# Performance work log

Hardware: AMD Instinct MI355X
Metric: run time of the kernel (lower is better)

## Reference

```python
import jax, jax.numpy as jnp
import numpy as np

B, N, HID, NH = 16, 200, 64, 2
D = HID // NH
EPS = 1e-12
LOG_EPS = 1e-24


def setup_inputs() -> dict:
    key = jax.random.key(0)
    ks = jax.random.split(key, 24)
    r = lambda k, shp, s=1.0: (jax.random.normal(k, shp, dtype=jnp.float32) * s)
    inp = {
        "input_tensor": r(ks[0], (B, N, HID), 0.5),
        "attention_mask": jnp.zeros((B, 1, N, N), jnp.float32),
        "absolute_pos_K": r(ks[1], (B, N, HID), 0.5),
        "absolute_pos_V": r(ks[2], (B, N, HID), 0.5),
        "time_matrix_emb_K": r(ks[3], (B, N, N, HID), 0.1),
        "time_matrix_emb_V": r(ks[4], (B, N, N, HID), 0.1),
        # learned params (torch nn.Linear convention: y = x @ W.T + b)
        "Wq": r(ks[5], (HID, HID), 0.02), "bq": jnp.zeros((HID,), jnp.float32),
        "Wk": r(ks[6], (HID, HID), 0.02), "bk": jnp.zeros((HID,), jnp.float32),
        "Wv": r(ks[7], (HID, HID), 0.02), "bv": jnp.zeros((HID,), jnp.float32),
        "Wd": r(ks[8], (HID, HID), 0.02), "bd": jnp.zeros((HID,), jnp.float32),
        "order_w": r(ks[9], (2 * D,), 0.02), "order_b": jnp.zeros((1,), jnp.float32),
        "dist_w": r(ks[10], (2 * D,), 0.02), "dist_b": jnp.zeros((1,), jnp.float32),
        "scalar": r(ks[11], (1,)),
        "ln_g": jnp.ones((HID,), jnp.float32), "ln_b": jnp.zeros((HID,), jnp.float32),
    }
    return inp


def _split_heads(x):  # [B,N,HID] -> [B,NH,N,D]
    return x.reshape(B, N, NH, D).transpose(0, 2, 1, 3)


def reference(input_tensor, attention_mask, absolute_pos_K, absolute_pos_V,
              time_matrix_emb_K, time_matrix_emb_V,
              Wq, bq, Wk, bk, Wv, bv, Wd, bd,
              order_w, order_b, dist_w, dist_b, scalar, ln_g, ln_b):
    q = _split_heads(input_tensor @ Wq.T + bq)   # [B,H,N,D]
    k = _split_heads(input_tensor @ Wk.T + bk)
    v = _split_heads(input_tensor @ Wv.T + bv)
    pk = _split_heads(absolute_pos_K)
    pv = _split_heads(absolute_pos_V)
    tk = time_matrix_emb_K.reshape(B, N, N, NH, D).transpose(0, 3, 1, 2, 4)  # [B,H,N,N,D]
    tv = time_matrix_emb_V.reshape(B, N, N, NH, D).transpose(0, 3, 1, 2, 4)

    scores = jnp.einsum('bhid,bhjd->bhij', q, k)
    scores = scores + jnp.einsum('bhid,bhjd->bhij', q, pk)
    scores = scores + jnp.einsum('bhijd,bhid->bhij', tk, q)

    # order term: order_affine(cat(q_i, k_j)) decomposes as q_i.w1 + k_j.w2 + b,
    # so we never materialize the [B,H,N,N,2D] q_k tensor.
    logit_o = (jnp.einsum('bhid,d->bhi', q, order_w[:D])[..., :, None]
               + jnp.einsum('bhjd,d->bhj', k, order_w[D:])[..., None, :]
               + order_b[0])
    pr_order = jax.nn.sigmoid(logit_o)
    gd_order = jnp.triu(jnp.ones((N, N), jnp.float32), 1)  # 1 where j > i
    err_order = (jnp.log(pr_order + LOG_EPS) * gd_order
                 + jnp.log(1.0 - pr_order + LOG_EPS) * (1.0 - gd_order))

    # distance term (same decomposition)
    pr_dist = (jnp.einsum('bhid,d->bhi', q, dist_w[:D])[..., :, None]
               + jnp.einsum('bhjd,d->bhj', k, dist_w[D:])[..., None, :]
               + dist_b[0])
    idx = jnp.arange(N)
    gd_dist = jnp.log(jnp.abs(idx[None, :] - idx[:, None]).astype(jnp.float32) + 1.0)
    err_dist = -jnp.square(gd_dist - pr_dist) * jnp.square(scalar[0]) * 0.5

    scores = (scores + err_order + err_dist) / np.sqrt(D).astype(np.float32)
    scores = scores + attention_mask
    probs = jax.nn.softmax(scores, axis=-1)  # dropout is identity in eval mode

    ctx = (jnp.einsum('bhij,bhjd->bhid', probs, v)
           + jnp.einsum('bhij,bhjd->bhid', probs, pv)
           + jnp.einsum('bhij,bhijd->bhid', probs, tv))
    ctx = ctx.transpose(0, 2, 1, 3).reshape(B, N, HID)

    h = ctx @ Wd.T + bd + input_tensor
    mu = h.mean(-1, keepdims=True)
    var = jnp.square(h - mu).mean(-1, keepdims=True)
    return (h - mu) / jnp.sqrt(var + EPS) * ln_g + ln_b
```

## Files before the change

kernel.cpp:

```cpp
#include <hip/hip_runtime.h>
#include <math.h>

#define B 16
#define N 200
#define HID 64
#define NH 2
#define D 32
#define EPSF 1e-12f
#define LOG_EPSF 1e-24f

#define RSQRT_D 0.17677669529663687f

__global__ __launch_bounds__(256) void k_proj(
    const float* __restrict__ x,
    const float* __restrict__ pk,
    const float* __restrict__ pv,
    const float* __restrict__ Wq, const float* __restrict__ bq,
    const float* __restrict__ Wk, const float* __restrict__ bk,
    const float* __restrict__ Wv, const float* __restrict__ bv,
    const float* __restrict__ order_w, const float* __restrict__ dist_w,
    float* __restrict__ q,
    float* __restrict__ kp,
    float* __restrict__ vp,
    float* __restrict__ qo, float* __restrict__ ko,
    float* __restrict__ qd, float* __restrict__ kd)
{
    __shared__ float sX[4][HID];
    const int tid = threadIdx.x;
    const int sub = tid >> 6;
    const int o   = tid & 63;
    const int row = blockIdx.x * 4 + sub;

    sX[sub][o] = x[row * HID + o];
    __syncthreads();

    float qv = bq[o], kv = bk[o], vv = bv[o];
    #pragma unroll 8
    for (int c = 0; c < HID; ++c) {
        const float xv = sX[sub][c];
        qv = fmaf(xv, Wq[o * HID + c], qv);
        kv = fmaf(xv, Wk[o * HID + c], kv);
        vv = fmaf(xv, Wv[o * HID + c], vv);
    }
    q [row * HID + o] = qv;
    kp[row * HID + o] = kv + pk[row * HID + o];
    vp[row * HID + o] = vv + pv[row * HID + o];

    const int d = o & 31;
    float qov = qv * order_w[d];
    float kov = kv * order_w[D + d];
    float qdv = qv * dist_w[d];
    float kdv = kv * dist_w[D + d];
    #pragma unroll
    for (int m = 16; m >= 1; m >>= 1) {
        qov += __shfl_xor(qov, m);
        kov += __shfl_xor(kov, m);
        qdv += __shfl_xor(qdv, m);
        kdv += __shfl_xor(kdv, m);
    }
    if (d == 0) {
        const int bb = row / N;
        const int ii = row - bb * N;
        const int h  = o >> 5;
        const int idx = (bb * NH + h) * N + ii;
        qo[idx] = qov;  ko[idx] = kov;
        qd[idx] = qdv;  kd[idx] = kdv;
    }
}

__global__ __launch_bounds__(128) void k_attn(
    const float* __restrict__ q, const float* __restrict__ kp,
    const float* __restrict__ vp,
    const float* __restrict__ tk,
    const float* __restrict__ tv,
    const float* __restrict__ amask,
    const float* __restrict__ qo, const float* __restrict__ ko,
    const float* __restrict__ qd, const float* __restrict__ kd,
    const float* __restrict__ order_b, const float* __restrict__ dist_b,
    const float* __restrict__ scalar,
    float* __restrict__ ctx)
{
    __shared__ float sS[2][256];

    const int tid  = threadIdx.x;
    const int h    = tid >> 6;
    const int lane = tid & 63;
    const int g    = lane >> 3;
    const int c    = lane & 7;
    const int bi   = blockIdx.x;
    const int b    = bi / N;
    const int i    = bi - b * N;
    const int bh   = b * NH + h;

    float* S = sS[h];

    const float4 qf = ((const float4*)(q + (size_t)bi * HID + h * D))[c];

    const float qoi = qo[bh * N + i];
    const float qdi = qd[bh * N + i];
    const float ob  = order_b[0];
    const float db  = dist_b[0];
    const float sc  = scalar[0];
    const float sc2h = 0.5f * sc * sc;

    const float* kpb = kp + (size_t)b * N * HID + h * D;
    const float* tkb = tk + (size_t)bi * N * HID + h * D;
    const float* vpb = vp + (size_t)b * N * HID + h * D;
    const float* tvb = tv + (size_t)bi * N * HID + h * D;
    const float* mb  = amask + (size_t)bi * N;
    const float* kob = ko + (size_t)bh * N;
    const float* kdb = kd + (size_t)bh * N;

    #pragma unroll 5
    for (int it = 0; it < 25; ++it) {
        const int j = it * 8 + g;
        const float4 kv  = ((const float4*)(kpb + (size_t)j * HID))[c];
        const float4 tkv = ((const float4*)(tkb + (size_t)j * HID))[c];
        float part = qf.x * (kv.x + tkv.x) + qf.y * (kv.y + tkv.y)
                   + qf.z * (kv.z + tkv.z) + qf.w * (kv.w + tkv.w);
        part += __shfl_xor(part, 1);
        part += __shfl_xor(part, 2);
        part += __shfl_xor(part, 4);

        const float lo = qoi + kob[j] + ob;
        const float pr = 1.0f / (1.0f + expf(-lo));
        const float eo = (j > i) ? logf(pr + LOG_EPSF) : logf(1.0f - pr + LOG_EPSF);
        const float pd = qdi + kdb[j] + db;
        const float gd = logf((float)(j > i ? j - i : i - j) + 1.0f);
        const float dv = gd - pd;
        const float ed = -sc2h * dv * dv;

        const float sj = (part + eo + ed) * RSQRT_D + mb[j];
        if (c == 0) S[j] = sj;
    }
    asm volatile("s_waitcnt lgkmcnt(0)" ::: "memory");

    const float s0 = S[lane];
    const float s1 = S[lane + 64];
    const float s2 = S[lane + 128];
    const float s3 = (lane < 8) ? S[lane + 192] : -INFINITY;
    float m = fmaxf(fmaxf(s0, s1), fmaxf(s2, s3));
    #pragma unroll
    for (int k = 32; k >= 1; k >>= 1) m = fmaxf(m, __shfl_xor(m, k));
    const float e0 = expf(s0 - m);
    const float e1 = expf(s1 - m);
    const float e2 = expf(s2 - m);
    const float e3 = (lane < 8) ? expf(s3 - m) : 0.0f;
    float t = e0 + e1 + e2 + e3;
    #pragma unroll
    for (int k = 32; k >= 1; k >>= 1) t += __shfl_xor(t, k);
    const float rinv = 1.0f / t;
    S[lane]       = e0 * rinv;
    S[lane + 64]  = e1 * rinv;
    S[lane + 128] = e2 * rinv;
    if (lane < 8) S[lane + 192] = e3 * rinv;
    asm volatile("s_waitcnt lgkmcnt(0)" ::: "memory");

    float4 r = make_float4(0.f, 0.f, 0.f, 0.f);
    #pragma unroll 5
    for (int it = 0; it < 25; ++it) {
        const int j = it * 8 + g;
        const float p = S[j];
        const float4 vv  = ((const float4*)(vpb + (size_t)j * HID))[c];
        const float4 tvv = ((const float4*)(tvb + (size_t)j * HID))[c];
        r.x += p * (vv.x + tvv.x);
        r.y += p * (vv.y + tvv.y);
        r.z += p * (vv.z + tvv.z);
        r.w += p * (vv.w + tvv.w);
    }
    #pragma unroll
    for (int k = 8; k <= 32; k <<= 1) {
        r.x += __shfl_xor(r.x, k);
        r.y += __shfl_xor(r.y, k);
        r.z += __shfl_xor(r.z, k);
        r.w += __shfl_xor(r.w, k);
    }
    if (g == 0)
        ((float4*)(ctx + (size_t)bi * HID + h * D))[c] = r;
}

__global__ __launch_bounds__(256) void k_out(
    const float* __restrict__ ctx, const float* __restrict__ x,
    const float* __restrict__ Wd, const float* __restrict__ bd,
    const float* __restrict__ ln_g, const float* __restrict__ ln_b,
    float* __restrict__ out)
{
    __shared__ float sC[4][HID];
    const int tid = threadIdx.x;
    const int sub = tid >> 6;
    const int o   = tid & 63;
    const int row = blockIdx.x * 4 + sub;

    sC[sub][o] = ctx[row * HID + o];
    __syncthreads();

    float hv = bd[o] + x[row * HID + o];
    #pragma unroll 8
    for (int c = 0; c < HID; ++c)
        hv = fmaf(sC[sub][c], Wd[o * HID + c], hv);

    float sum = hv;
    #pragma unroll
    for (int m = 32; m >= 1; m >>= 1) sum += __shfl_xor(sum, m);
    const float mu = sum * (1.0f / 64.0f);
    const float dv = hv - mu;
    float vs = dv * dv;
    #pragma unroll
    for (int m = 32; m >= 1; m >>= 1) vs += __shfl_xor(vs, m);
    const float var = vs * (1.0f / 64.0f);

    out[row * HID + o] = dv * rsqrtf(var + EPSF) * ln_g[o] + ln_b[o];
}

extern "C" void kernel_launch(void* const* d_in, const int* in_sizes, int n_in,
                              void* d_out, int out_size, void* d_ws, size_t ws_size,
                              hipStream_t stream) {
    const float* x     = (const float*)d_in[0];
    const float* amask = (const float*)d_in[1];
    const float* apk   = (const float*)d_in[2];
    const float* apv   = (const float*)d_in[3];
    const float* tk    = (const float*)d_in[4];
    const float* tv    = (const float*)d_in[5];
    const float* Wq    = (const float*)d_in[6];
    const float* bq    = (const float*)d_in[7];
    const float* Wk    = (const float*)d_in[8];
    const float* bk    = (const float*)d_in[9];
    const float* Wv    = (const float*)d_in[10];
    const float* bv    = (const float*)d_in[11];
    const float* Wd    = (const float*)d_in[12];
    const float* bd    = (const float*)d_in[13];
    const float* order_w = (const float*)d_in[14];
    const float* order_b = (const float*)d_in[15];
    const float* dist_w  = (const float*)d_in[16];
    const float* dist_b  = (const float*)d_in[17];
    const float* scalar  = (const float*)d_in[18];
    const float* ln_g    = (const float*)d_in[19];
    const float* ln_b    = (const float*)d_in[20];

    float* ws = (float*)d_ws;
    const size_t nrow = (size_t)B * N * HID;
    float* qbuf  = ws;
    float* kpbuf = ws + nrow;
    float* vpbuf = ws + 2 * nrow;
    float* ctxb  = ws + 3 * nrow;
    float* qob   = ws + 4 * nrow;
    float* kob   = qob + (size_t)B * NH * N;
    float* qdb   = kob + (size_t)B * NH * N;
    float* kdb   = qdb + (size_t)B * NH * N;

    k_proj<<<(B * N) / 4, 256, 0, stream>>>(x, apk, apv, Wq, bq, Wk, bk, Wv, bv,
                                            order_w, dist_w,
                                            qbuf, kpbuf, vpbuf, qob, kob, qdb, kdb);

    k_attn<<<B * N, 128, 0, stream>>>(qbuf, kpbuf, vpbuf, tk, tv, amask,
                                      qob, kob, qdb, kdb,
                                      order_b, dist_b, scalar, ctxb);

    k_out<<<(B * N) / 4, 256, 0, stream>>>(ctxb, x, Wd, bd, ln_g, ln_b,
                                           (float*)d_out);
}
```

Baseline: 114.7 us.

## Split attention per head into 64-thread blocks and compute aux terms lane-parallel

Each attention block now handles one (batch, head, query) triple with a single wavefront instead of two heads per 128-thread block, doubling the grid size. The order and distance bias terms are moved out of the 8-lane-group dot loop into a separate lane-parallel pass, so each score is computed once per lane rather than redundantly across 8 lanes. The sigmoid-log is rewritten as a softplus (-log1p(exp(x))). The goal is to cut redundant transcendental work and give the scheduler more independent wavefronts. The cost is extra shared-memory traffic and a changed epsilon behaviour in the log term.

```diff
diff --git a/kernel.cpp b/kernel.cpp
--- a/kernel.cpp
+++ b/kernel.cpp
@@ -68,7 +68,7 @@
     }
 }
 
-__global__ __launch_bounds__(128) void k_attn(
+__global__ __launch_bounds__(64) void k_attn(
     const float* __restrict__ q, const float* __restrict__ kp,
     const float* __restrict__ vp,
     const float* __restrict__ tk,
@@ -80,19 +80,18 @@
     const float* __restrict__ scalar,
     float* __restrict__ ctx)
 {
-    __shared__ float sS[2][256];
-
-    const int tid  = threadIdx.x;
-    const int h    = tid >> 6;
-    const int lane = tid & 63;
+    __shared__ float S_aux[256];
+    __shared__ float S_dot[256];
+
+    const int lane = threadIdx.x;
     const int g    = lane >> 3;
     const int c    = lane & 7;
-    const int bi   = blockIdx.x;
-    const int b    = bi / N;
-    const int i    = bi - b * N;
-    const int bh   = b * NH + h;
-
-    float* S = sS[h];
+    const int bid  = blockIdx.x;
+    const int bh   = bid / N;
+    const int i    = bid - bh * N;
+    const int b    = bh >> 1;
+    const int h    = bh & 1;
+    const int bi   = b * N + i;
 
     const float4 qf = ((const float4*)(q + (size_t)bi * HID + h * D))[c];
 
@@ -110,6 +109,20 @@
     const float* mb  = amask + (size_t)bi * N;
     const float* kob = ko + (size_t)bh * N;
     const float* kdb = kd + (size_t)bh * N;
+
+    #pragma unroll
+    for (int r = 0; r < 4; ++r) {
+        const int j = r * 64 + lane;
+        if (j < N) {
+            const float lo = qoi + kob[j] + ob;
+            const float xs = (j > i) ? -lo : lo;
+            const float eo = -log1pf(expf(xs));
+            const float pd = qdi + kdb[j] + db;
+            const float gd = logf((float)(j > i ? j - i : i - j) + 1.0f);
+            const float dv = gd - pd;
+            S_aux[j] = (eo - sc2h * dv * dv) * RSQRT_D + mb[j];
+        }
+    }
 
     #pragma unroll 5
     for (int it = 0; it < 25; ++it) {
@@ -121,24 +134,14 @@
         part += __shfl_xor(part, 1);
         part += __shfl_xor(part, 2);
         part += __shfl_xor(part, 4);
-
-        const float lo = qoi + kob[j] + ob;
-        const float pr = 1.0f / (1.0f + expf(-lo));
-        const float eo = (j > i) ? logf(pr + LOG_EPSF) : logf(1.0f - pr + LOG_EPSF);
-        const float pd = qdi + kdb[j] + db;
-        const float gd = logf((float)(j > i ? j - i : i - j) + 1.0f);
-        const float dv = gd - pd;
-        const float ed = -sc2h * dv * dv;
-
-        const float sj = (part + eo + ed) * RSQRT_D + mb[j];
-        if (c == 0) S[j] = sj;
+        if (c == 0) S_dot[j] = part * RSQRT_D;
     }
     asm volatile("s_waitcnt lgkmcnt(0)" ::: "memory");
 
-    const float s0 = S[lane];
-    const float s1 = S[lane + 64];
-    const float s2 = S[lane + 128];
-    const float s3 = (lane < 8) ? S[lane + 192] : -INFINITY;
+    const float s0 = S_aux[lane]       + S_dot[lane];
+    const float s1 = S_aux[lane + 64]  + S_dot[lane + 64];
+    const float s2 = S_aux[lane + 128] + S_dot[lane + 128];
+    const float s3 = (lane < 8) ? (S_aux[lane + 192] + S_dot[lane + 192]) : -INFINITY;
     float m = fmaxf(fmaxf(s0, s1), fmaxf(s2, s3));
     #pragma unroll
     for (int k = 32; k >= 1; k >>= 1) m = fmaxf(m, __shfl_xor(m, k));
@@ -150,33 +153,33 @@
     #pragma unroll
     for (int k = 32; k >= 1; k >>= 1) t += __shfl_xor(t, k);
     const float rinv = 1.0f / t;
-    S[lane]       = e0 * rinv;
-    S[lane + 64]  = e1 * rinv;
-    S[lane + 128] = e2 * rinv;
-    if (lane < 8) S[lane + 192] = e3 * rinv;
+    S_aux[lane]       = e0 * rinv;
+    S_aux[lane + 64]  = e1 * rinv;
+    S_aux[lane + 128] = e2 * rinv;
+    if (lane < 8) S_aux[lane + 192] = e3 * rinv;
     asm volatile("s_waitcnt lgkmcnt(0)" ::: "memory");
 
-    float4 r = make_float4(0.f, 0.f, 0.f, 0.f);
+    float4 r4 = make_float4(0.f, 0.f, 0.f, 0.f);
     #pragma unroll 5
     for (int it = 0; it < 25; ++it) {
         const int j = it * 8 + g;
-        const float p = S[j];
+        const float p = S_aux[j];
         const float4 vv  = ((const float4*)(vpb + (size_t)j * HID))[c];
         const float4 tvv = ((const float4*)(tvb + (size_t)j * HID))[c];
-        r.x += p * (vv.x + tvv.x);
-        r.y += p * (vv.y + tvv.y);
-        r.z += p * (vv.z + tvv.z);
-        r.w += p * (vv.w + tvv.w);
+        r4.x += p * (vv.x + tvv.x);
+        r4.y += p * (vv.y + tvv.y);
+        r4.z += p * (vv.z + tvv.z);
+        r4.w += p * (vv.w + tvv.w);
     }
     #pragma unroll
     for (int k = 8; k <= 32; k <<= 1) {
-        r.x += __shfl_xor(r.x, k);
-        r.y += __shfl_xor(r.y, k);
-        r.z += __shfl_xor(r.z, k);
-        r.w += __shfl_xor(r.w, k);
+        r4.x += __shfl_xor(r4.x, k);
+        r4.y += __shfl_xor(r4.y, k);
+        r4.z += __shfl_xor(r4.z, k);
+        r4.w += __shfl_xor(r4.w, k);
     }
     if (g == 0)
-        ((float4*)(ctx + (size_t)bi * HID + h * D))[c] = r;
+        ((float4*)(ctx + (size_t)bi * HID + h * D))[c] = r4;
 }
 
 __global__ __launch_bounds__(256) void k_out(
@@ -252,9 +255,9 @@
                                             order_w, dist_w,
                                             qbuf, kpbuf, vpbuf, qob, kob, qdb, kdb);
 
-    k_attn<<<B * N, 128, 0, stream>>>(qbuf, kpbuf, vpbuf, tk, tv, amask,
-                                      qob, kob, qdb, kdb,
-                                      order_b, dist_b, scalar, ctxb);
+    k_attn<<<B * NH * N, 64, 0, stream>>>(qbuf, kpbuf, vpbuf, tk, tv, amask,
+                                          qob, kob, qdb, kdb,
+                                          order_b, dist_b, scalar, ctxb);
 
     k_out<<<(B * N) / 4, 256, 0, stream>>>(ctxb, x, Wd, bd, ln_g, ln_b,
                                            (float*)d_out);
```

Result: faster. 106.7 us, median of 2 (-7.0%).
